# Kernel optimization log

Measured on AMD Instinct MI355X. Metric: run time of the kernel, lower is better.

The kernel has to match this reference:

```python
import jax, jax.numpy as jnp
import numpy as np

V_REST = 0.0
V_RESET = 0.0
V_TH = 1.27
TAU = 50.0
SPIKE_DURATION = 1
SCALE = 100.0  # SurrGradSpike.scale


@jax.custom_vjp
def spike(x):
    return (x > 0).astype(x.dtype)

def _spike_fwd(x):
    return (x > 0).astype(x.dtype), x

def _spike_bwd(x, g):
    # normalized negative part of fast sigmoid (Zenke & Ganguli 2018)
    return (g / (SCALE * jnp.abs(x) + 1.0) ** 2,)

spike.defvjp(_spike_fwd, _spike_bwd)


def _shift(a, k):
    # a[:, j] -> a[:, j + k], zero padded out of range
    if k == 0:
        return a
    if k > 0:
        return jnp.pad(a[:, k:], ((0, 0), (0, k)))
    return jnp.pad(a[:, :k], ((0, 0), (-k, 0)))


def _lif(ode, decay):
    ode2 = ode[..., 0]          # [B, T]
    B, T = ode2.shape
    ode_t = ode2.T              # [T, B] for scan

    def step(carry, inp):
        v, counter, z = carry   # z = remaining steps whose dv reads are zeroed
        t, x = inp
        v = v - decay * (v - V_REST)
        v = jnp.where(counter == 1, V_RESET, v)
        # dv[:, t] was zeroed by a spike within the previous 5 steps (torch in-place window)
        x_eff = jnp.where(z > 0, 0.0, x)
        v = v + x_eff
        v = jnp.where(counter > 1, V_TH, v)
        s = spike(v - V_TH)
        s_d = jax.lax.stop_gradient(s)
        counter = counter + (SPIKE_DURATION + 1) * s_d
        v = jnp.where(counter > 1, V_TH, v)
        # spike at t zeroes dv[:, t-1:t+6]; at t==0 the torch slice [-1:6] is empty
        z = jnp.where((s_d > 0) & (t >= 1), 5.0, jnp.maximum(z - 1.0, 0.0))
        counter = jnp.maximum(counter - 1.0, 0.0)
        return (v, counter, z), (v, s, s_d)

    v0 = jnp.full((B,), V_REST, dtype=ode2.dtype)
    c0 = jnp.zeros((B,), dtype=ode2.dtype)
    z0 = jnp.zeros((B,), dtype=ode2.dtype)
    ts = jnp.arange(T)
    _, (v_rec, s_rec, sd_rec) = jax.lax.scan(step, (v0, c0, z0), (ts, ode_t))
    v_rec = v_rec.T             # [B, T]
    s_rec = s_rec.T             # [B, T]

    sp = sd_rec.T > 0           # detached spike mask [B, T]
    sp = sp.at[:, 0].set(False)  # spike at t=0 zeroes nothing (empty slice in torch)
    # column j of dv is zeroed iff a spike occurred at t' in [j-5, j+1]
    zero_mask = jnp.zeros_like(sp)
    for k in range(-5, 2):
        zero_mask = zero_mask | _shift(sp, k)
    dv = jnp.where(zero_mask, 0.0, ode2)
    return v_rec, s_rec, dv


def setup_inputs() -> dict:
    key = jax.random.key(0)
    B, T = 2048, 4096
    ode = jax.random.normal(key, (B, T, 1), dtype=jnp.float32)
    decay = jnp.float32(1.0 / TAU)  # LIF.decay parameter (learn_tau=False)
    return {"ode": ode, "decay": decay}


def reference(ode, decay):
    return _lif(ode, decay)
```

## Files before the change

### kernel.cpp

```cpp
#include <hip/hip_runtime.h>

constexpr int   T   = 4096;
constexpr float VTH = 1.27f;
constexpr int   K   = 32;
constexpr int   L   = T / K;
constexpr int   LG  = L / 4;
constexpr int   WG  = 160;

__device__ __forceinline__ bool sstep(float x, float decay, float& v, unsigned& h, bool& gate) {
    float t1 = __fmul_rn(decay, v);
    float vd = __fsub_rn(v, t1);
    float xe = gate ? 0.0f : x;
    float vn = __fadd_rn(vd, xe);
    bool  s  = vn > VTH;
    v = s ? 0.0f : vn;
    bool g4 = (h & 15u) != 0u;
    h = (h << 1) | (s ? 1u : 0u);
    gate = s || g4;
    return s;
}

__device__ __forceinline__ bool ostep(float x, float decay, float& v, unsigned& h, bool& gate,
                                      float& vo, float& so, float& dvo, float xprev) {
    float t1 = __fmul_rn(decay, v);
    float vd = __fsub_rn(v, t1);
    float xe = gate ? 0.0f : x;
    float vn = __fadd_rn(vd, xe);
    bool  s  = vn > VTH;
    vo = s ? VTH  : vn;
    so = s ? 1.0f : 0.0f;
    v  = s ? 0.0f : vn;
    bool z6 = s || ((h & 63u) != 0u);
    dvo = z6 ? 0.0f : xprev;
    bool g4 = (h & 15u) != 0u;
    h = (h << 1) | (s ? 1u : 0u);
    gate = s || g4;
    return s;
}

__device__ __forceinline__ void ogroup(float4 X, float decay, float& v, unsigned& h, bool& gate,
                                       float& xprev, float4& vo, float4& so,
                                       float& close, float& px, float& py, float& pz) {
    ostep(X.x, decay, v, h, gate, vo.x, so.x, close, xprev); xprev = X.x;
    ostep(X.y, decay, v, h, gate, vo.y, so.y, px,    xprev); xprev = X.y;
    ostep(X.z, decay, v, h, gate, vo.z, so.z, py,    xprev); xprev = X.z;
    ostep(X.w, decay, v, h, gate, vo.w, so.w, pz,    xprev); xprev = X.w;
}

__global__ __launch_bounds__(256)
void xt_pass(const float* __restrict__ ode, float4* __restrict__ xT, int B) {
    __shared__ float4 tile[64][8];
    const int tid = threadIdx.x;
    const int ntt = T / 32;
    const int tt  = blockIdx.x % ntt;
    const int rb  = (blockIdx.x / ntt) * 64;
    const int g0  = tt * 8;
    const float4* __restrict__ x4g = (const float4*)ode;

    {
        int r = tid >> 3, c = tid & 7;
        tile[r][c ^ (r & 7)]           = x4g[(size_t)(rb + r)      * (T / 4) + g0 + c];
        int r2 = r + 32;
        tile[r2][c ^ (r2 & 7)]         = x4g[(size_t)(rb + r2)     * (T / 4) + g0 + c];
    }
    __syncthreads();
    {
        int l = tid & 63, j = tid >> 6;
        size_t obase = ((size_t)(rb >> 6) * (T / 4) + g0) * 64;
        xT[obase + (size_t)j       * 64 + l] = tile[l][j       ^ (l & 7)];
        xT[obase + (size_t)(j + 4) * 64 + l] = tile[l][(j + 4) ^ (l & 7)];
    }
}

__device__ __forceinline__ void flush_pair(int p, int tid, int rb, int k,
        float* __restrict__ vout, float* __restrict__ sout, float* __restrict__ dvout,
        const float4 (*tv)[8], const float4 (*ts)[8], const float4 (*td)[64][8]) {
    __syncthreads();
    const int cc = (tid & 7) ^ (tid >> 3);
#pragma unroll
    for (int jj = 0; jj < 8; ++jj) {
        int rr = jj * 8 + (tid >> 3);
        size_t off = (size_t)(rb + rr) * T + k * L + p * 32 + (tid & 7) * 4;
        *(float4*)(vout + off) = tv[rr][cc];
        *(float4*)(sout + off) = ts[rr][cc];
        if (p >= 1) *(float4*)(dvout + off - 32) = td[(p - 1) & 1][rr][cc];
    }
    __syncthreads();
}

__global__ __launch_bounds__(64, 1)
void lif_spec(const float4* __restrict__ xT, const float* __restrict__ decay_p,
              float* __restrict__ vout, float* __restrict__ sout, float* __restrict__ dvout,
              float2* __restrict__ Sst, float2* __restrict__ Est, int B) {
    __shared__ float4 tv[64][8];
    __shared__ float4 ts[64][8];
    __shared__ float4 td[2][64][8];

    const int tid = threadIdx.x;
    const int gg  = blockIdx.x * 64;
    const int rb  = gg % B;
    const int k   = gg / B;
    const int b   = rb + tid;
    const float decay = decay_p[0];
    const int xs7 = tid & 7;

    const size_t xb = (size_t)(rb >> 6) * (T / 4) * 64 + tid;
#define XLD(g) xT[xb + (size_t)(g) * 64]

    const int g0f = k * LG;
    const int wg  = (k == 0) ? 0 : (k * LG < WG ? k * LG : WG);
    float v = 0.0f; unsigned h = 0u; bool gate = false;
    float xprev = 0.0f;

    if (wg > 0) {
        const size_t xwb = xb + (size_t)(g0f - wg) * 64;
        const bool t0row = (g0f - wg == 0);
        float4 Q[16];
#pragma unroll
        for (int i = 0; i < 16; ++i) Q[i] = xT[xwb + (size_t)i * 64];
        for (int c = 0; c < wg; c += 16) {
#pragma unroll
            for (int i = 0; i < 16; ++i) {
                if (i == 0 && c == 0 && t0row) {
                    sstep(Q[0].x, decay, v, h, gate); h = 0u; gate = false;
                    sstep(Q[0].y, decay, v, h, gate);
                    sstep(Q[0].z, decay, v, h, gate);
                    sstep(Q[0].w, decay, v, h, gate);
                } else {
                    sstep(Q[i].x, decay, v, h, gate);
                    sstep(Q[i].y, decay, v, h, gate);
                    sstep(Q[i].z, decay, v, h, gate);
                    sstep(Q[i].w, decay, v, h, gate);
                }
                Q[i] = xT[xwb + (size_t)(c + i + 16) * 64];
            }
        }
        Sst[k * B + b] = make_float2(v, __uint_as_float(h & 127u));
    }

    float4 A0 = XLD(g0f),     A1 = XLD(g0f + 1), A2 = XLD(g0f + 2), A3 = XLD(g0f + 3);
    float4 B0 = XLD(g0f + 4), B1 = XLD(g0f + 5), B2 = XLD(g0f + 6), B3 = XLD(g0f + 7);
    float4 Pd;

#define OG(X, gidx) { float4 V_, S_; float cl_, p0_, p1_, p2_; \
        ogroup(X, decay, v, h, gate, xprev, V_, S_, cl_, p0_, p1_, p2_); \
        if ((gidx) > 0) { Pd.w = cl_; \
            td[(((gidx) - 1) >> 3) & 1][tid][(((gidx) - 1) & 7) ^ xs7] = Pd; } \
        Pd.x = p0_; Pd.y = p1_; Pd.z = p2_; \
        tv[tid][((gidx) & 7) ^ xs7] = V_; ts[tid][((gidx) & 7) ^ xs7] = S_; }

    {
        if (k == 0) {
            float4 V_, S_; float dvd;
            bool s0 = ostep(A0.x, decay, v, h, gate, V_.x, S_.x, dvd, xprev); xprev = A0.x;
            h = 0u; gate = false;
            bool s1 = ostep(A0.y, decay, v, h, gate, V_.y, S_.y, Pd.x, xprev); xprev = A0.y;
            ostep(A0.z, decay, v, h, gate, V_.z, S_.z, Pd.y, xprev); xprev = A0.z;
            ostep(A0.w, decay, v, h, gate, V_.w, S_.w, Pd.z, xprev); xprev = A0.w;
            if (s0 && s1) V_.z = VTH;
            tv[tid][xs7] = V_; ts[tid][xs7] = S_;
        } else {
            float4 V_, S_; float cl_;
            ogroup(A0, decay, v, h, gate, xprev, V_, S_, cl_, Pd.x, Pd.y, Pd.z);
            tv[tid][xs7] = V_; ts[tid][xs7] = S_;
        }
        A0 = XLD(g0f + 8);
        OG(A1, 1) A1 = XLD(g0f + 9);
        OG(A2, 2) A2 = XLD(g0f + 10);
        OG(A3, 3) A3 = XLD(g0f + 11);
        OG(B0, 4) B0 = XLD(g0f + 12);
        OG(B1, 5) B1 = XLD(g0f + 13);
        OG(B2, 6) B2 = XLD(g0f + 14);
        OG(B3, 7) B3 = XLD(g0f + 15);
        flush_pair(0, tid, rb, k, vout, sout, dvout, tv, ts, td);
    }
    OG(A0, 8)  A0 = XLD(g0f + 16); OG(A1, 9)  A1 = XLD(g0f + 17);
    OG(A2, 10) A2 = XLD(g0f + 18); OG(A3, 11) A3 = XLD(g0f + 19);
    OG(B0, 12) B0 = XLD(g0f + 20); OG(B1, 13) B1 = XLD(g0f + 21);
    OG(B2, 14) B2 = XLD(g0f + 22); OG(B3, 15) B3 = XLD(g0f + 23);
    flush_pair(1, tid, rb, k, vout, sout, dvout, tv, ts, td);
    OG(A0, 16) A0 = XLD(g0f + 24); OG(A1, 17) A1 = XLD(g0f + 25);
    OG(A2, 18) A2 = XLD(g0f + 26); OG(A3, 19) A3 = XLD(g0f + 27);
    OG(B0, 20) B0 = XLD(g0f + 28); OG(B1, 21) B1 = XLD(g0f + 29);
    OG(B2, 22) B2 = XLD(g0f + 30); OG(B3, 23) B3 = XLD(g0f + 31);
    flush_pair(2, tid, rb, k, vout, sout, dvout, tv, ts, td);
    OG(A0, 24) OG(A1, 25) OG(A2, 26) OG(A3, 27)
    OG(B0, 28) OG(B1, 29) OG(B2, 30) OG(B3, 31)
    flush_pair(3, tid, rb, k, vout, sout, dvout, tv, ts, td);
#undef OG

    Est[k * B + b] = make_float2(v, __uint_as_float(h & 127u));

    if (k < K - 1) {
        float xla = XLD((k + 1) * LG).x;
        float vo_, so_;
        ostep(xla, decay, v, h, gate, vo_, so_, Pd.w, xprev);
    } else {
        Pd.w = ((h & 63u) != 0u) ? 0.0f : xprev;
    }
    td[1][tid][7 ^ xs7] = Pd;
    __syncthreads();
    {
        const int cc = (tid & 7) ^ (tid >> 3);
#pragma unroll
        for (int jj = 0; jj < 8; ++jj) {
            int rr = jj * 8 + (tid >> 3);
            size_t off = (size_t)(rb + rr) * T + k * L + 3 * 32 + (tid & 7) * 4;
            *(float4*)(dvout + off) = td[1][rr][cc];
        }
    }
#undef XLD
}

__global__ __launch_bounds__(64, 1)
void lif_fix(const float* __restrict__ ode, const float* __restrict__ decay_p,
             float* __restrict__ vout, float* __restrict__ sout, float* __restrict__ dvout,
             const float2* __restrict__ Sst, const float2* __restrict__ Est, int B) {
    const int b = blockIdx.x * 64 + threadIdx.x;
    const float decay = decay_p[0];

    float2 E  = Est[b];
    float2 S1 = Sst[B + b];
    float2 E1 = Est[B + b];
    for (int k = 1; k < K; ++k) {
        float2 S = S1, Ek = E1;
        if (k + 1 < K) { S1 = Sst[(k + 1) * B + b]; E1 = Est[(k + 1) * B + b]; }
        bool match = (S.x == E.x) && (__float_as_uint(S.y) == __float_as_uint(E.y));
        if (match) { E = Ek; continue; }

        const size_t bt = (size_t)b * T;
        const float4* __restrict__ x4 = (const float4*)(ode + bt);
        float4* __restrict__ v4 = (float4*)(vout + bt);
        float4* __restrict__ s4 = (float4*)(sout + bt);
        float4* __restrict__ d4 = (float4*)(dvout + bt);
        const int g0f = k * LG;

        float v = E.x; unsigned h = __float_as_uint(E.y);
        bool gate = (h & 31u) != 0u;
        float xprev = 0.0f;
        float4 pend;

        float4 Q0 = x4[g0f], Q1 = x4[g0f + 1], Q2 = x4[g0f + 2], Q3 = x4[g0f + 3];
        {
            float4 vo, so; float cl;
            ogroup(Q0, decay, v, h, gate, xprev, vo, so, cl, pend.x, pend.y, pend.z);
            v4[g0f] = vo; s4[g0f] = so;
            Q0 = x4[g0f + 4];
        }
#define FPROC(cc, Q) { float4 vo, so; float px, py, pz; \
            ogroup(Q, decay, v, h, gate, xprev, vo, so, pend.w, px, py, pz); \
            d4[g0f + (cc) - 1] = pend; \
            pend.x = px; pend.y = py; pend.z = pz; \
            v4[g0f + (cc)] = vo; s4[g0f + (cc)] = so; }
        FPROC(1, Q1) Q1 = x4[g0f + 5];
        FPROC(2, Q2) Q2 = x4[g0f + 6];
        FPROC(3, Q3) Q3 = x4[g0f + 7];
        for (int c0 = 4; c0 < LG; c0 += 4) {
            FPROC(c0,     Q0) Q0 = x4[g0f + (c0 + 4 < LG ? c0 + 4 : LG - 1)];
            FPROC(c0 + 1, Q1) Q1 = x4[g0f + (c0 + 5 < LG ? c0 + 5 : LG - 1)];
            FPROC(c0 + 2, Q2) Q2 = x4[g0f + (c0 + 6 < LG ? c0 + 6 : LG - 1)];
            FPROC(c0 + 3, Q3) Q3 = x4[g0f + (c0 + 7 < LG ? c0 + 7 : LG - 1)];
        }
#undef FPROC
        E = make_float2(v, __uint_as_float(h & 127u));
        if (k < K - 1) {
            float xla = ode[bt + (size_t)(k + 1) * L];
            float vo_, so_;
            ostep(xla, decay, v, h, gate, vo_, so_, pend.w, xprev);
        } else {
            pend.w = ((h & 63u) != 0u) ? 0.0f : xprev;
        }
        d4[g0f + LG - 1] = pend;
    }
}

extern "C" void kernel_launch(void* const* d_in, const int* in_sizes, int n_in,
                              void* d_out, int out_size, void* d_ws, size_t ws_size,
                              hipStream_t stream) {
    const float* ode   = (const float*)d_in[0];
    const float* decay = (const float*)d_in[1];
    float* out = (float*)d_out;

    const int BT = in_sizes[0];
    const int B  = BT / T;

    float* vout  = out;
    float* sout  = out + (size_t)BT;
    float* dvout = out + 2 * (size_t)BT;

    float2* Sst = (float2*)d_ws;
    float2* Est = Sst + (size_t)K * B;
    float4* xT  = (float4*)((char*)d_ws + 2 * (size_t)K * B * sizeof(float2));

    xt_pass<<<dim3((T / 32) * (B / 64)), dim3(256), 0, stream>>>(ode, xT, B);
    lif_spec<<<dim3((B * K) / 64), dim3(64), 0, stream>>>(xT, decay, vout, sout, dvout,
                                                          Sst, Est, B);
    lif_fix<<<dim3(B / 64), dim3(64), 0, stream>>>(ode, decay, vout, sout, dvout,
                                                   Sst, Est, B);
}
```

Before: 184.2 us.

## Drop transpose pass; stage input tiles into LDS via global_load_lds

Removes the separate xt_pass kernel that transposed the input into a workspace, and has lif_spec read the original row-major input directly. Each 8-group chunk is staged into shared memory with the direct global-to-LDS load builtin, software-pipelined one chunk ahead using explicit vmcnt/lgkmcnt waits. The block-wide barriers in the flush are replaced with wait-count instructions, which the single-wavefront block makes sufficient. This saves a full read and write of the input plus a kernel launch, at the cost of a hand-tuned wait-count scheme that is fragile.

```diff
diff --git a/kernel.cpp b/kernel.cpp
--- a/kernel.cpp
+++ b/kernel.cpp
@@ -5,7 +5,7 @@
 constexpr int   K   = 32;
 constexpr int   L   = T / K;
 constexpr int   LG  = L / 4;
-constexpr int   WG  = 160;
+constexpr int   WGG = 160;
 
 __device__ __forceinline__ bool sstep(float x, float decay, float& v, unsigned& h, bool& gate) {
     float t1 = __fmul_rn(decay, v);
@@ -47,35 +47,26 @@
     ostep(X.w, decay, v, h, gate, vo.w, so.w, pz,    xprev); xprev = X.w;
 }
 
-__global__ __launch_bounds__(256)
-void xt_pass(const float* __restrict__ ode, float4* __restrict__ xT, int B) {
-    __shared__ float4 tile[64][8];
-    const int tid = threadIdx.x;
-    const int ntt = T / 32;
-    const int tt  = blockIdx.x % ntt;
-    const int rb  = (blockIdx.x / ntt) * 64;
-    const int g0  = tt * 8;
-    const float4* __restrict__ x4g = (const float4*)ode;
-
-    {
-        int r = tid >> 3, c = tid & 7;
-        tile[r][c ^ (r & 7)]           = x4g[(size_t)(rb + r)      * (T / 4) + g0 + c];
-        int r2 = r + 32;
-        tile[r2][c ^ (r2 & 7)]         = x4g[(size_t)(rb + r2)     * (T / 4) + g0 + c];
-    }
-    __syncthreads();
-    {
-        int l = tid & 63, j = tid >> 6;
-        size_t obase = ((size_t)(rb >> 6) * (T / 4) + g0) * 64;
-        xT[obase + (size_t)j       * 64 + l] = tile[l][j       ^ (l & 7)];
-        xT[obase + (size_t)(j + 4) * 64 + l] = tile[l][(j + 4) ^ (l & 7)];
-    }
+#define WVM(N) do { asm volatile("s_waitcnt vmcnt(" #N ")" ::: "memory"); \
+                    __builtin_amdgcn_sched_barrier(0); } while (0)
+#define WLG()  do { asm volatile("s_waitcnt lgkmcnt(0)" ::: "memory"); \
+                    __builtin_amdgcn_sched_barrier(0); } while (0)
+
+using GU32 = const __attribute__((address_space(1))) unsigned int;
+using LU32 = __attribute__((address_space(3))) unsigned int;
+
+__device__ __forceinline__ void stage8(const float* src0, float4* lbuf) {
+    LU32* lp = (LU32*)lbuf;
+#pragma unroll
+    for (int j = 0; j < 8; ++j)
+        __builtin_amdgcn_global_load_lds((GU32*)(src0 + (size_t)j * 8 * T),
+                                         lp + j * 256, 16, 0, 0);
 }
 
 __device__ __forceinline__ void flush_pair(int p, int tid, int rb, int k,
         float* __restrict__ vout, float* __restrict__ sout, float* __restrict__ dvout,
         const float4 (*tv)[8], const float4 (*ts)[8], const float4 (*td)[64][8]) {
-    __syncthreads();
+    WLG();
     const int cc = (tid & 7) ^ (tid >> 3);
 #pragma unroll
     for (int jj = 0; jj < 8; ++jj) {
@@ -85,13 +76,14 @@
         *(float4*)(sout + off) = ts[rr][cc];
         if (p >= 1) *(float4*)(dvout + off - 32) = td[(p - 1) & 1][rr][cc];
     }
-    __syncthreads();
+    WLG();
 }
 
 __global__ __launch_bounds__(64, 1)
-void lif_spec(const float4* __restrict__ xT, const float* __restrict__ decay_p,
+void lif_spec(const float* __restrict__ ode, const float* __restrict__ decay_p,
               float* __restrict__ vout, float* __restrict__ sout, float* __restrict__ dvout,
               float2* __restrict__ Sst, float2* __restrict__ Est, int B) {
+    __shared__ float4 xin[64 * 8];
     __shared__ float4 tv[64][8];
     __shared__ float4 ts[64][8];
     __shared__ float4 td[2][64][8];
@@ -104,42 +96,43 @@
     const float decay = decay_p[0];
     const int xs7 = tid & 7;
 
-    const size_t xb = (size_t)(rb >> 6) * (T / 4) * 64 + tid;
-#define XLD(g) xT[xb + (size_t)(g) * 64]
-
     const int g0f = k * LG;
-    const int wg  = (k == 0) ? 0 : (k * LG < WG ? k * LG : WG);
+    const int wgg = (k == 0) ? 0 : (g0f < WGG ? g0f : WGG);
+    const int nw  = wgg >> 3;
+    const int gstart = g0f - wgg;
+
     float v = 0.0f; unsigned h = 0u; bool gate = false;
     float xprev = 0.0f;
 
-    if (wg > 0) {
-        const size_t xwb = xb + (size_t)(g0f - wg) * 64;
-        const bool t0row = (g0f - wg == 0);
-        float4 Q[16];
-#pragma unroll
-        for (int i = 0; i < 16; ++i) Q[i] = xT[xwb + (size_t)i * 64];
-        for (int c = 0; c < wg; c += 16) {
-#pragma unroll
-            for (int i = 0; i < 16; ++i) {
-                if (i == 0 && c == 0 && t0row) {
-                    sstep(Q[0].x, decay, v, h, gate); h = 0u; gate = false;
-                    sstep(Q[0].y, decay, v, h, gate);
-                    sstep(Q[0].z, decay, v, h, gate);
-                    sstep(Q[0].w, decay, v, h, gate);
-                } else {
-                    sstep(Q[i].x, decay, v, h, gate);
-                    sstep(Q[i].y, decay, v, h, gate);
-                    sstep(Q[i].z, decay, v, h, gate);
-                    sstep(Q[i].w, decay, v, h, gate);
-                }
-                Q[i] = xT[xwb + (size_t)(c + i + 16) * 64];
-            }
-        }
-        Sst[k * B + b] = make_float2(v, __uint_as_float(h & 127u));
-    }
-
-    float4 A0 = XLD(g0f),     A1 = XLD(g0f + 1), A2 = XLD(g0f + 2), A3 = XLD(g0f + 3);
-    float4 B0 = XLD(g0f + 4), B1 = XLD(g0f + 5), B2 = XLD(g0f + 6), B3 = XLD(g0f + 7);
+    float xla = (k < K - 1) ? ode[(size_t)b * T + (size_t)(k + 1) * L] : 0.0f;
+
+#define STAGE(t) stage8(ode + ((size_t)(rb + (tid >> 3)) * T \
+                               + (size_t)(gstart + 8 * (t)) * 4 + (tid & 7) * 4), xin)
+#define RD8 const float4* xr = xin + (size_t)tid * 8; \
+            float4 G0 = xr[0], G1 = xr[1], G2 = xr[2], G3 = xr[3], \
+                   G4 = xr[4], G5 = xr[5], G6 = xr[6], G7 = xr[7];
+#define WG4(G) { sstep(G.x, decay, v, h, gate); sstep(G.y, decay, v, h, gate); \
+                 sstep(G.z, decay, v, h, gate); sstep(G.w, decay, v, h, gate); }
+
+    STAGE(0);
+
+    if (nw > 0) {
+        const bool t0row = (gstart == 0);
+        for (int t = 0; t < nw; ++t) {
+            WVM(0);
+            RD8
+            WLG();
+            STAGE(t + 1);
+            if (t == 0 && t0row) {
+                sstep(G0.x, decay, v, h, gate); h = 0u; gate = false;
+                sstep(G0.y, decay, v, h, gate);
+                sstep(G0.z, decay, v, h, gate);
+                sstep(G0.w, decay, v, h, gate);
+            } else { WG4(G0) }
+            WG4(G1) WG4(G2) WG4(G3) WG4(G4) WG4(G5) WG4(G6) WG4(G7)
+        }
+    }
+
     float4 Pd;
 
 #define OG(X, gidx) { float4 V_, S_; float cl_, p0_, p1_, p2_; \
@@ -150,56 +143,68 @@
         tv[tid][((gidx) & 7) ^ xs7] = V_; ts[tid][((gidx) & 7) ^ xs7] = S_; }
 
     {
+        WVM(0);
+        RD8
+        WLG();
+        STAGE(nw + 1);
+        if (nw > 0) Sst[k * B + b] = make_float2(v, __uint_as_float(h & 127u));
         if (k == 0) {
             float4 V_, S_; float dvd;
-            bool s0 = ostep(A0.x, decay, v, h, gate, V_.x, S_.x, dvd, xprev); xprev = A0.x;
+            bool s0 = ostep(G0.x, decay, v, h, gate, V_.x, S_.x, dvd, xprev); xprev = G0.x;
             h = 0u; gate = false;
-            bool s1 = ostep(A0.y, decay, v, h, gate, V_.y, S_.y, Pd.x, xprev); xprev = A0.y;
-            ostep(A0.z, decay, v, h, gate, V_.z, S_.z, Pd.y, xprev); xprev = A0.z;
-            ostep(A0.w, decay, v, h, gate, V_.w, S_.w, Pd.z, xprev); xprev = A0.w;
+            bool s1 = ostep(G0.y, decay, v, h, gate, V_.y, S_.y, Pd.x, xprev); xprev = G0.y;
+            ostep(G0.z, decay, v, h, gate, V_.z, S_.z, Pd.y, xprev); xprev = G0.z;
+            ostep(G0.w, decay, v, h, gate, V_.w, S_.w, Pd.z, xprev); xprev = G0.w;
             if (s0 && s1) V_.z = VTH;
             tv[tid][xs7] = V_; ts[tid][xs7] = S_;
         } else {
             float4 V_, S_; float cl_;
-            ogroup(A0, decay, v, h, gate, xprev, V_, S_, cl_, Pd.x, Pd.y, Pd.z);
+            ogroup(G0, decay, v, h, gate, xprev, V_, S_, cl_, Pd.x, Pd.y, Pd.z);
             tv[tid][xs7] = V_; ts[tid][xs7] = S_;
         }
-        A0 = XLD(g0f + 8);
-        OG(A1, 1) A1 = XLD(g0f + 9);
-        OG(A2, 2) A2 = XLD(g0f + 10);
-        OG(A3, 3) A3 = XLD(g0f + 11);
-        OG(B0, 4) B0 = XLD(g0f + 12);
-        OG(B1, 5) B1 = XLD(g0f + 13);
-        OG(B2, 6) B2 = XLD(g0f + 14);
-        OG(B3, 7) B3 = XLD(g0f + 15);
+        OG(G1, 1) OG(G2, 2) OG(G3, 3) OG(G4, 4) OG(G5, 5) OG(G6, 6) OG(G7, 7)
         flush_pair(0, tid, rb, k, vout, sout, dvout, tv, ts, td);
     }
-    OG(A0, 8)  A0 = XLD(g0f + 16); OG(A1, 9)  A1 = XLD(g0f + 17);
-    OG(A2, 10) A2 = XLD(g0f + 18); OG(A3, 11) A3 = XLD(g0f + 19);
-    OG(B0, 12) B0 = XLD(g0f + 20); OG(B1, 13) B1 = XLD(g0f + 21);
-    OG(B2, 14) B2 = XLD(g0f + 22); OG(B3, 15) B3 = XLD(g0f + 23);
-    flush_pair(1, tid, rb, k, vout, sout, dvout, tv, ts, td);
-    OG(A0, 16) A0 = XLD(g0f + 24); OG(A1, 17) A1 = XLD(g0f + 25);
-    OG(A2, 18) A2 = XLD(g0f + 26); OG(A3, 19) A3 = XLD(g0f + 27);
-    OG(B0, 20) B0 = XLD(g0f + 28); OG(B1, 21) B1 = XLD(g0f + 29);
-    OG(B2, 22) B2 = XLD(g0f + 30); OG(B3, 23) B3 = XLD(g0f + 31);
-    flush_pair(2, tid, rb, k, vout, sout, dvout, tv, ts, td);
-    OG(A0, 24) OG(A1, 25) OG(A2, 26) OG(A3, 27)
-    OG(B0, 28) OG(B1, 29) OG(B2, 30) OG(B3, 31)
-    flush_pair(3, tid, rb, k, vout, sout, dvout, tv, ts, td);
+    {
+        WVM(16);
+        RD8
+        WLG();
+        STAGE(nw + 2);
+        OG(G0, 8)  OG(G1, 9)  OG(G2, 10) OG(G3, 11)
+        OG(G4, 12) OG(G5, 13) OG(G6, 14) OG(G7, 15)
+        flush_pair(1, tid, rb, k, vout, sout, dvout, tv, ts, td);
+    }
+    {
+        WVM(24);
+        RD8
+        WLG();
+        STAGE(nw + 3);
+        OG(G0, 16) OG(G1, 17) OG(G2, 18) OG(G3, 19)
+        OG(G4, 20) OG(G5, 21) OG(G6, 22) OG(G7, 23)
+        flush_pair(2, tid, rb, k, vout, sout, dvout, tv, ts, td);
+    }
+    {
+        WVM(24);
+        RD8
+        OG(G0, 24) OG(G1, 25) OG(G2, 26) OG(G3, 27)
+        OG(G4, 28) OG(G5, 29) OG(G6, 30) OG(G7, 31)
+        flush_pair(3, tid, rb, k, vout, sout, dvout, tv, ts, td);
+    }
 #undef OG
+#undef RD8
+#undef WG4
+#undef STAGE
 
     Est[k * B + b] = make_float2(v, __uint_as_float(h & 127u));
 
     if (k < K - 1) {
-        float xla = XLD((k + 1) * LG).x;
         float vo_, so_;
         ostep(xla, decay, v, h, gate, vo_, so_, Pd.w, xprev);
     } else {
         Pd.w = ((h & 63u) != 0u) ? 0.0f : xprev;
     }
     td[1][tid][7 ^ xs7] = Pd;
-    __syncthreads();
+    WLG();
     {
         const int cc = (tid & 7) ^ (tid >> 3);
 #pragma unroll
@@ -209,7 +214,6 @@
             *(float4*)(dvout + off) = td[1][rr][cc];
         }
     }
-#undef XLD
 }
 
 __global__ __launch_bounds__(64, 1)
@@ -290,10 +294,8 @@
 
     float2* Sst = (float2*)d_ws;
     float2* Est = Sst + (size_t)K * B;
-    float4* xT  = (float4*)((char*)d_ws + 2 * (size_t)K * B * sizeof(float2));
-
-    xt_pass<<<dim3((T / 32) * (B / 64)), dim3(256), 0, stream>>>(ode, xT, B);
-    lif_spec<<<dim3((B * K) / 64), dim3(64), 0, stream>>>(xT, decay, vout, sout, dvout,
+
+    lif_spec<<<dim3((B * K) / 64), dim3(64), 0, stream>>>(ode, decay, vout, sout, dvout,
                                                           Sst, Est, B);
     lif_fix<<<dim3(B / 64), dim3(64), 0, stream>>>(ode, decay, vout, sout, dvout,
                                                    Sst, Est, B);
```

Measured after the change: 171.4 us. 6.9% less time.
